# Kernel optimization log

Hardware: AMD Instinct MI355X
Metric: run time of the kernel (lower is better)

## Reference

```python
import jax, jax.numpy as jnp
import numpy as np

B, S, H = 2, 2048, 2048
NH, NKV, HD = 16, 4, 128
SCALING = HD ** -0.5


def rotate_half(x):
    x1, x2 = jnp.split(x, 2, axis=-1)
    return jnp.concatenate((-x2, x1), axis=-1)


def apply_rope(t, cos, sin):
    # t: [B, nh, S, HD]; cos/sin: [B, S, HD] -> unsqueeze head dim
    c = cos[:, None, :, :]
    s = sin[:, None, :, :]
    return t * c + rotate_half(t) * s


def setup_inputs() -> dict:
    key = jax.random.key(0)
    k1, k2, k3, k4, k5 = jax.random.split(key, 5)
    hidden_states = jax.random.normal(k1, (B, S, H), dtype=jnp.float32)
    # real RoPE tables
    inv_freq = 1.0 / (10000.0 ** (jnp.arange(0, HD, 2, dtype=jnp.float32) / HD))
    pos = jnp.arange(S, dtype=jnp.float32)
    freqs = jnp.einsum('s,d->sd', pos, inv_freq)              # [S, HD/2]
    emb = jnp.concatenate((freqs, freqs), axis=-1)            # [S, HD]
    cos = jnp.broadcast_to(jnp.cos(emb)[None], (B, S, HD))
    sin = jnp.broadcast_to(jnp.sin(emb)[None], (B, S, HD))
    # additive causal mask [B, 1, S, S]
    causal = jnp.triu(jnp.full((S, S), -1e9, dtype=jnp.float32), k=1)
    attention_mask = jnp.broadcast_to(causal[None, None], (B, 1, S, S))
    sc = 0.02
    wq = jax.random.normal(k2, (NH * HD, H), dtype=jnp.float32) * sc
    wk = jax.random.normal(k3, (NKV * HD, H), dtype=jnp.float32) * sc
    wv = jax.random.normal(k4, (NKV * HD, H), dtype=jnp.float32) * sc
    wo = jax.random.normal(k5, (H, NH * HD), dtype=jnp.float32) * sc
    return {"hidden_states": hidden_states, "cos": cos, "sin": sin,
            "attention_mask": attention_mask, "wq": wq, "wk": wk, "wv": wv, "wo": wo}


def reference(hidden_states, cos, sin, attention_mask, wq, wk, wv, wo):
    x = hidden_states
    # fused-style QKV projections (nn.Linear: x @ W.T), split heads -> [B, nh, S, HD]
    q = (x @ wq.T).reshape(B, S, NH, HD).transpose(0, 2, 1, 3)
    k = (x @ wk.T).reshape(B, S, NKV, HD).transpose(0, 2, 1, 3)
    v = (x @ wv.T).reshape(B, S, NKV, HD).transpose(0, 2, 1, 3)
    q = apply_rope(q, cos, sin)
    k = apply_rope(k, cos, sin)
    # GQA: repeat KV heads (repeat_kv)
    n_rep = NH // NKV
    k = jnp.repeat(k, n_rep, axis=1)
    v = jnp.repeat(v, n_rep, axis=1)
    scores = jnp.einsum('bhqd,bhkd->bhqk', q, k) * SCALING + attention_mask
    attn = jax.nn.softmax(scores.astype(jnp.float32), axis=-1).astype(q.dtype)
    out = jnp.einsum('bhqk,bhkd->bhqd', attn, v)
    out = out.transpose(0, 2, 1, 3).reshape(B, S, NH * HD)
    out = out @ wo.T
    return (out, attn)
```

## Files before the change

### kernel.cpp

```cpp
#include <hip/hip_runtime.h>
#include <cstdint>
#include <cstddef>

typedef __bf16 bf16;
typedef __attribute__((ext_vector_type(8))) __bf16 bf16x8;
typedef __attribute__((ext_vector_type(4))) __bf16 bf16x4;
typedef __attribute__((ext_vector_type(4))) float f32x4;

constexpr int B_ = 2, S_ = 2048, H_ = 2048, NH_ = 16, NKV_ = 4, HD_ = 128;
constexpr float SCALE_ = 0.08838834764831845f;

#define GLDS16(g, l)                                                        \
  __builtin_amdgcn_global_load_lds(                                         \
      (const __attribute__((address_space(1))) void*)(g),                   \
      (__attribute__((address_space(3))) void*)(l), 16, 0, 0)

#define VMCNT0 asm volatile("s_waitcnt vmcnt(0)" ::: "memory")
#define VMCNT4 asm volatile("s_waitcnt vmcnt(4)" ::: "memory")
#define VMCNT8 asm volatile("s_waitcnt vmcnt(8)" ::: "memory")
#define BAR __builtin_amdgcn_s_barrier()

__global__ void cvt_all(const float* __restrict__ hs, const float* __restrict__ wq,
                        const float* __restrict__ wk, const float* __restrict__ wv,
                        const float* __restrict__ wo, bf16* __restrict__ xb,
                        bf16* __restrict__ w3b, bf16* __restrict__ wob) {
  const int stride = gridDim.x * blockDim.x;
  for (int i = blockIdx.x * blockDim.x + threadIdx.x; i < 4718592; i += stride) {
    const float4* s; bf16x4* d; int j;
    if (i < 2097152)      { s = (const float4*)hs; d = (bf16x4*)xb;            j = i; }
    else if (i < 3145728) { s = (const float4*)wq; d = (bf16x4*)w3b;           j = i - 2097152; }
    else if (i < 3407872) { s = (const float4*)wk; d = (bf16x4*)w3b + 1048576; j = i - 3145728; }
    else if (i < 3670016) { s = (const float4*)wv; d = (bf16x4*)w3b + 1310720; j = i - 3407872; }
    else                  { s = (const float4*)wo; d = (bf16x4*)wob;           j = i - 3670016; }
    float4 v = s[j];
    bf16x4 o;
    o[0] = (bf16)v.x; o[1] = (bf16)v.y; o[2] = (bf16)v.z; o[3] = (bf16)v.w;
    d[j] = o;
  }
}

template <int EPI>
__global__ __launch_bounds__(256, 2) void gemm_bt(const bf16* __restrict__ A,
                                                  const bf16* __restrict__ Bm, int K,
                                                  bf16* __restrict__ qb, bf16* __restrict__ kb,
                                                  bf16* __restrict__ vtb, float* __restrict__ Cout) {
  __shared__ __align__(16) bf16 As[2][128 * 64];
  __shared__ __align__(16) bf16 Bs[2][128 * 64];
  const int tid = threadIdx.x;
  const int lane = tid & 63;
  const int wid = tid >> 6;
  const int fid = blockIdx.y * 32 + blockIdx.x;
  const int nwg = gridDim.y * 32;
  const int swz = (fid & 7) * (nwg >> 3) + (fid >> 3);
  const int m0 = (swz & 31) * 128;
  const int n0 = (swz >> 5) * 128;
  const int wm = (wid >> 1) * 64, wn = (wid & 1) * 64;
  const int r = lane & 15, g = lane >> 4;
  f32x4 acc[4][4] = {};

  auto STAGE = [&](int kt, int cc) {
#pragma unroll
    for (int i = 0; i < 4; ++i) {
      int cb = wid * 256 + i * 64;
      int c64 = cb + lane;
      int row = c64 >> 3, cs = (c64 & 7) ^ (row & 7);
      GLDS16(A + (size_t)(m0 + row) * K + kt + cs * 8, &As[cc][cb * 8]);
      GLDS16(Bm + (size_t)(n0 + row) * K + kt + cs * 8, &Bs[cc][cb * 8]);
    }
  };

  STAGE(0, 0);
  int c = 0;
#pragma unroll 1
  for (int kt = 0; kt < K; kt += 64) {
    if (kt + 64 < K) {
      STAGE(kt + 64, c ^ 1);
      VMCNT8;
    } else {
      VMCNT0;
    }
    BAR;
#pragma unroll
    for (int ks = 0; ks < 2; ++ks) {
      bf16x8 af[4], bfr[4];
#pragma unroll
      for (int fm = 0; fm < 4; ++fm)
        af[fm] = *(const bf16x8*)(&As[c][(wm + fm * 16 + r) * 64 + (((ks * 4 + g) ^ (r & 7)) << 3)]);
#pragma unroll
      for (int fn = 0; fn < 4; ++fn)
        bfr[fn] = *(const bf16x8*)(&Bs[c][(wn + fn * 16 + r) * 64 + (((ks * 4 + g) ^ (r & 7)) << 3)]);
#pragma unroll
      for (int fm = 0; fm < 4; ++fm)
#pragma unroll
        for (int fn = 0; fn < 4; ++fn)
          acc[fm][fn] = __builtin_amdgcn_mfma_f32_16x16x32_bf16(af[fm], bfr[fn], acc[fm][fn], 0, 0, 0);
    }
    BAR;
    c ^= 1;
  }

#pragma unroll
  for (int fm = 0; fm < 4; ++fm)
#pragma unroll
    for (int fn = 0; fn < 4; ++fn)
#pragma unroll
      for (int rr = 0; rr < 4; ++rr) {
        int mm = m0 + wm + fm * 16 + g * 4 + rr;
        int nn = n0 + wn + fn * 16 + r;
        float v = acc[fm][fn][rr];
        if (EPI == 1) {
          Cout[(size_t)mm * 2048 + nn] = v;
        } else {
          int b = mm >> 11, s = mm & (S_ - 1);
          int d = nn & 127;
          if (nn < 2048) {
            int hh = nn >> 7;
            qb[(((size_t)b * NH_ + hh) * S_ + s) * HD_ + d] = (bf16)v;
          } else if (nn < 2560) {
            int hh = (nn - 2048) >> 7;
            kb[(((size_t)b * NKV_ + hh) * S_ + s) * HD_ + d] = (bf16)v;
          } else {
            int hh = (nn - 2560) >> 7;
            vtb[(((size_t)b * NKV_ + hh) * HD_ + d) * S_ + s] = (bf16)v;
          }
        }
      }
}

__global__ void rope_kernel(bf16* __restrict__ qb, bf16* __restrict__ kb,
                            const float* __restrict__ cosp, const float* __restrict__ sinp) {
  const int NQ = B_ * NH_ * S_;
  const int NK = B_ * NKV_ * S_;
  const int tot = (NQ + NK) * 8;
  int t = blockIdx.x * blockDim.x + threadIdx.x;
  if (t >= tot) return;
  const int oct = t & 7, rid = t >> 3;
  bf16* base;
  int b, s;
  if (rid < NQ) {
    base = qb + (size_t)rid * HD_;
    s = rid & (S_ - 1);
    b = rid >> 15;
  } else {
    int r2 = rid - NQ;
    base = kb + (size_t)r2 * HD_;
    s = r2 & (S_ - 1);
    b = r2 >> 13;
  }
  const int d = oct * 8;
  const float* cp = cosp + ((size_t)b * S_ + s) * HD_ + d;
  const float* sp = sinp + ((size_t)b * S_ + s) * HD_ + d;
  float4 c0 = *(const float4*)cp, c1 = *(const float4*)(cp + 4);
  float4 s0 = *(const float4*)sp, s1 = *(const float4*)(sp + 4);
  float cc[8] = {c0.x, c0.y, c0.z, c0.w, c1.x, c1.y, c1.z, c1.w};
  float ss[8] = {s0.x, s0.y, s0.z, s0.w, s1.x, s1.y, s1.z, s1.w};
  bf16x8 x1 = *(const bf16x8*)(base + d);
  bf16x8 x2 = *(const bf16x8*)(base + d + 64);
  bf16x8 o1, o2;
#pragma unroll
  for (int i = 0; i < 8; ++i) {
    float a = (float)x1[i], bb = (float)x2[i];
    o1[i] = (bf16)(a * cc[i] - bb * ss[i]);
    o2[i] = (bf16)(bb * cc[i] + a * ss[i]);
  }
  *(bf16x8*)(base + d) = o1;
  *(bf16x8*)(base + d + 64) = o2;
}

__global__ __launch_bounds__(256, 2) void attn_kernel(const bf16* __restrict__ qb,
                                                      const bf16* __restrict__ kb,
                                                      const bf16* __restrict__ vtb,
                                                      bf16* __restrict__ aob,
                                                      float* __restrict__ attn_out) {
  __shared__ __align__(16) bf16 Ks[2][64 * 128];
  __shared__ __align__(16) bf16 Vs[2][128 * 64];
  __shared__ __align__(16) bf16 Ps[64 * 64];
  const int bid = (blockIdx.x & 7) * 64 + (blockIdx.x >> 3);
  const int p = bid & 15;
  const int h = (bid >> 4) & 15;
  const int b = bid >> 8;
  const int kh = h >> 2;
  const int tid = threadIdx.x, lane = tid & 63, wid = tid >> 6;
  const int r = lane & 15, g = lane >> 4;

  const bf16* kbase = kb + ((size_t)b * NKV_ + kh) * S_ * HD_;
  const bf16* vbase = vtb + ((size_t)b * NKV_ + kh) * (size_t)HD_ * S_;
  const size_t ahead = (size_t)(b * NH_ + h) * S_;

  auto stageK = [&](int kt, int cc) {
#pragma unroll
    for (int i = 0; i < 4; ++i) {
      int base = i * 256 + wid * 64;
      int idx = base + lane;
      int row = idx >> 4, ch = (idx & 15) ^ (row & 7);
      GLDS16(kbase + (size_t)(kt * 64 + row) * HD_ + ch * 8, &Ks[cc][base * 8]);
    }
  };
  auto stageV = [&](int kt, int cc) {
#pragma unroll
    for (int i = 0; i < 4; ++i) {
      int base = i * 256 + wid * 64;
      int idx = base + lane;
      int row = idx >> 3, ch = (idx & 7) ^ (row & 7);
      GLDS16(vbase + (size_t)row * S_ + kt * 64 + ch * 8, &Vs[cc][base * 8]);
    }
  };

  int zc = 0;

#pragma unroll 1
  for (int sbi = 0; sbi < 2; ++sbi) {
    const int qt = sbi ? 31 - p : p;
    const int q0 = qt * 64;
    const int nt = qt + 1;
    const bf16* qsrc = qb + ((size_t)(b * NH_ + h) * S_ + q0) * HD_;

    bf16x8 qreg[4];
#pragma unroll
    for (int ks = 0; ks < 4; ++ks)
      qreg[ks] = *(const bf16x8*)(qsrc + (wid * 16 + r) * HD_ + ks * 32 + g * 8);

    float lsum = 0.f;
    stageK(0, 0);
    VMCNT0; BAR;
    int c = 0;
#pragma unroll 1
    for (int kt = 0; kt < nt; ++kt) {
      if (kt + 1 < nt) stageK(kt + 1, c ^ 1);
      const bool dz = (zc <= 30);
      if (dz) {
        int qtz, ktz;
        if (zc < 31 - p) { qtz = p; ktz = p + 1 + zc; }
        else             { qtz = 31 - p; ktz = zc + 1; }
        float* zdst = attn_out + (ahead + qtz * 64) * S_ + ktz * 64;
        float4 z = {0.f, 0.f, 0.f, 0.f};
#pragma unroll
        for (int i = 0; i < 4; ++i) {
          int idx = i * 256 + tid;
          *(float4*)(zdst + (size_t)(idx >> 4) * S_ + (idx & 15) * 4) = z;
        }
        ++zc;
      }
      f32x4 sacc[4] = {};
      __builtin_amdgcn_s_setprio(1);
#pragma unroll
      for (int ks = 0; ks < 4; ++ks)
#pragma unroll
        for (int fn = 0; fn < 4; ++fn) {
          bf16x8 kk = *(const bf16x8*)(&Ks[c][(fn * 16 + r) * 128 + (((ks * 4 + g) ^ (r & 7)) << 3)]);
          sacc[fn] = __builtin_amdgcn_mfma_f32_16x16x32_bf16(kk, qreg[ks], sacc[fn], 0, 0, 0);
        }
      __builtin_amdgcn_s_setprio(0);
      float ts = 0.f;
      if (kt == nt - 1) {
#pragma unroll
        for (int fn = 0; fn < 4; ++fn)
#pragma unroll
          for (int rr = 0; rr < 4; ++rr) {
            bool msk = (fn * 16 + g * 4 + rr) > (wid * 16 + r);
            ts += msk ? 0.f : __expf(sacc[fn][rr] * SCALE_);
          }
      } else {
#pragma unroll
        for (int fn = 0; fn < 4; ++fn)
#pragma unroll
          for (int rr = 0; rr < 4; ++rr) ts += __expf(sacc[fn][rr] * SCALE_);
      }
      ts += __shfl_xor(ts, 16);
      ts += __shfl_xor(ts, 32);
      lsum += ts;
      if (dz) { VMCNT4; } else { VMCNT0; }
      BAR;
      c ^= 1;
    }
    const float rl = 1.0f / lsum;

    f32x4 oacc[8] = {};
    const size_t arow0 = (ahead + q0) * S_;
    stageK(0, 0);
    stageV(0, 0);
    VMCNT0; BAR;
    c = 0;
#pragma unroll 1
    for (int kt = 0; kt < nt; ++kt) {
      if (kt + 1 < nt) { stageK(kt + 1, c ^ 1); stageV(kt + 1, c ^ 1); }
      const int k0 = kt * 64;
      f32x4 sacc[4] = {};
      __builtin_amdgcn_s_setprio(1);
#pragma unroll
      for (int ks = 0; ks < 4; ++ks)
#pragma unroll
        for (int fn = 0; fn < 4; ++fn) {
          bf16x8 kk = *(const bf16x8*)(&Ks[c][(fn * 16 + r) * 128 + (((ks * 4 + g) ^ (r & 7)) << 3)]);
          sacc[fn] = __builtin_amdgcn_mfma_f32_16x16x32_bf16(kk, qreg[ks], sacc[fn], 0, 0, 0);
        }
      __builtin_amdgcn_s_setprio(0);
      const int prow = (wid * 16 + r) * 64;
      if (kt == nt - 1) {
#pragma unroll
        for (int fn = 0; fn < 4; ++fn) {
          bf16x4 pk;
#pragma unroll
          for (int rr = 0; rr < 4; ++rr) {
            bool msk = (fn * 16 + g * 4 + rr) > (wid * 16 + r);
            pk[rr] = (bf16)(msk ? 0.f : __expf(sacc[fn][rr] * SCALE_) * rl);
          }
          *(bf16x4*)(&Ps[prow + ((((fn << 1) | (g >> 1)) ^ (r & 7)) << 3) + ((g & 1) << 2)]) = pk;
        }
      } else {
#pragma unroll
        for (int fn = 0; fn < 4; ++fn) {
          bf16x4 pk;
#pragma unroll
          for (int rr = 0; rr < 4; ++rr)
            pk[rr] = (bf16)(__expf(sacc[fn][rr] * SCALE_) * rl);
          *(bf16x4*)(&Ps[prow + ((((fn << 1) | (g >> 1)) ^ (r & 7)) << 3) + ((g & 1) << 2)]) = pk;
        }
      }
      {
        const int trow = tid >> 2, tcb = (tid & 3) * 16;
        float* dst = attn_out + arow0 + (size_t)trow * S_ + k0 + tcb;
        int ch0 = (tid & 3) * 2;
        bf16x8 p0 = *(const bf16x8*)(&Ps[trow * 64 + ((ch0 ^ (trow & 7)) << 3)]);
        bf16x8 p1 = *(const bf16x8*)(&Ps[trow * 64 + (((ch0 + 1) ^ (trow & 7)) << 3)]);
        float4 o0 = {(float)p0[0], (float)p0[1], (float)p0[2], (float)p0[3]};
        float4 o1 = {(float)p0[4], (float)p0[5], (float)p0[6], (float)p0[7]};
        float4 o2 = {(float)p1[0], (float)p1[1], (float)p1[2], (float)p1[3]};
        float4 o3 = {(float)p1[4], (float)p1[5], (float)p1[6], (float)p1[7]};
        *(float4*)(dst) = o0;
        *(float4*)(dst + 4) = o1;
        *(float4*)(dst + 8) = o2;
        *(float4*)(dst + 12) = o3;
      }
      __builtin_amdgcn_s_setprio(1);
#pragma unroll
      for (int ks = 0; ks < 2; ++ks) {
        bf16x8 pa = *(const bf16x8*)(&Ps[prow + (((ks * 4 + g) ^ (r & 7)) << 3)]);
#pragma unroll
        for (int fn = 0; fn < 8; ++fn) {
          bf16x8 vv = *(const bf16x8*)(&Vs[c][(fn * 16 + r) * 64 + (((ks * 4 + g) ^ (r & 7)) << 3)]);
          oacc[fn] = __builtin_amdgcn_mfma_f32_16x16x32_bf16(pa, vv, oacc[fn], 0, 0, 0);
        }
      }
      __builtin_amdgcn_s_setprio(0);
      VMCNT4; BAR;
      c ^= 1;
    }

#pragma unroll
    for (int fn = 0; fn < 8; ++fn)
#pragma unroll
      for (int rr = 0; rr < 4; ++rr) {
        int q = q0 + wid * 16 + g * 4 + rr;
        aob[((size_t)b * S_ + q) * 2048 + h * HD_ + fn * 16 + r] = (bf16)oacc[fn][rr];
      }
  }
}

extern "C" void kernel_launch(void* const* d_in, const int* in_sizes, int n_in,
                              void* d_out, int out_size, void* d_ws, size_t ws_size,
                              hipStream_t stream) {
  const float* hidden = (const float*)d_in[0];
  const float* cosp = (const float*)d_in[1];
  const float* sinp = (const float*)d_in[2];
  const float* wq = (const float*)d_in[4];
  const float* wk = (const float*)d_in[5];
  const float* wv = (const float*)d_in[6];
  const float* wo = (const float*)d_in[7];
  float* out = (float*)d_out;
  float* attn = out + (size_t)B_ * S_ * H_;

  char* ws = (char*)d_ws;
  bf16* xb  = (bf16*)(ws);
  bf16* w3b = (bf16*)(ws + (16ull << 20));
  bf16* wob = (bf16*)(ws + (28ull << 20));
  bf16* qb  = (bf16*)(ws + (36ull << 20));
  bf16* kb  = (bf16*)(ws + (52ull << 20));
  bf16* vtb = (bf16*)(ws + (56ull << 20));
  bf16* aob = (bf16*)(ws + (60ull << 20));

  cvt_all<<<2048, 256, 0, stream>>>(hidden, wq, wk, wv, wo, xb, w3b, wob);
  gemm_bt<0><<<dim3(32, 24), 256, 0, stream>>>(xb, w3b, 2048, qb, kb, vtb, nullptr);
  rope_kernel<<<2560, 256, 0, stream>>>(qb, kb, cosp, sinp);
  attn_kernel<<<512, 256, 0, stream>>>(qb, kb, vtb, aob, attn);
  gemm_bt<1><<<dim3(32, 16), 256, 0, stream>>>(aob, wob, 2048, nullptr, nullptr, nullptr, out);
}
```

Baseline: 349.7 us.

## Fuse Q RoPE into attention and single-buffer the projection GEMM

RoPE for Q is now applied in registers inside the attention kernel when the Q fragments are loaded, and the standalone rope kernel only rotates K. This removes a full read-modify-write pass over the Q tensor. Separately, the GEMM drops its double-buffered LDS pipeline for a single buffer with a full wait and two barriers per k-step, and relaxes the launch bounds. That halves LDS use but gives up overlap of global loads with MFMA work.

```diff
diff --git a/kernel.cpp b/kernel.cpp
--- a/kernel.cpp
+++ b/kernel.cpp
@@ -17,7 +17,6 @@
 
 #define VMCNT0 asm volatile("s_waitcnt vmcnt(0)" ::: "memory")
 #define VMCNT4 asm volatile("s_waitcnt vmcnt(4)" ::: "memory")
-#define VMCNT8 asm volatile("s_waitcnt vmcnt(8)" ::: "memory")
 #define BAR __builtin_amdgcn_s_barrier()
 
 __global__ void cvt_all(const float* __restrict__ hs, const float* __restrict__ wq,
@@ -40,12 +39,12 @@
 }
 
 template <int EPI>
-__global__ __launch_bounds__(256, 2) void gemm_bt(const bf16* __restrict__ A,
-                                                  const bf16* __restrict__ Bm, int K,
-                                                  bf16* __restrict__ qb, bf16* __restrict__ kb,
-                                                  bf16* __restrict__ vtb, float* __restrict__ Cout) {
-  __shared__ __align__(16) bf16 As[2][128 * 64];
-  __shared__ __align__(16) bf16 Bs[2][128 * 64];
+__global__ __launch_bounds__(256) void gemm_bt(const bf16* __restrict__ A,
+                                               const bf16* __restrict__ Bm, int K,
+                                               bf16* __restrict__ qb, bf16* __restrict__ kb,
+                                               bf16* __restrict__ vtb, float* __restrict__ Cout) {
+  __shared__ __align__(16) bf16 As[128 * 64];
+  __shared__ __align__(16) bf16 Bs[128 * 64];
   const int tid = threadIdx.x;
   const int lane = tid & 63;
   const int wid = tid >> 6;
@@ -58,45 +57,34 @@
   const int r = lane & 15, g = lane >> 4;
   f32x4 acc[4][4] = {};
 
-  auto STAGE = [&](int kt, int cc) {
+#pragma unroll 1
+  for (int kt = 0; kt < K; kt += 64) {
+    __syncthreads();
 #pragma unroll
     for (int i = 0; i < 4; ++i) {
       int cb = wid * 256 + i * 64;
       int c64 = cb + lane;
       int row = c64 >> 3, cs = (c64 & 7) ^ (row & 7);
-      GLDS16(A + (size_t)(m0 + row) * K + kt + cs * 8, &As[cc][cb * 8]);
-      GLDS16(Bm + (size_t)(n0 + row) * K + kt + cs * 8, &Bs[cc][cb * 8]);
-    }
-  };
-
-  STAGE(0, 0);
-  int c = 0;
-#pragma unroll 1
-  for (int kt = 0; kt < K; kt += 64) {
-    if (kt + 64 < K) {
-      STAGE(kt + 64, c ^ 1);
-      VMCNT8;
-    } else {
-      VMCNT0;
-    }
-    BAR;
+      GLDS16(A + (size_t)(m0 + row) * K + kt + cs * 8, As + cb * 8);
+      GLDS16(Bm + (size_t)(n0 + row) * K + kt + cs * 8, Bs + cb * 8);
+    }
+    VMCNT0;
+    __syncthreads();
 #pragma unroll
     for (int ks = 0; ks < 2; ++ks) {
       bf16x8 af[4], bfr[4];
 #pragma unroll
       for (int fm = 0; fm < 4; ++fm)
-        af[fm] = *(const bf16x8*)(&As[c][(wm + fm * 16 + r) * 64 + (((ks * 4 + g) ^ (r & 7)) << 3)]);
+        af[fm] = *(const bf16x8*)(As + (wm + fm * 16 + r) * 64 + (((ks * 4 + g) ^ (r & 7)) << 3));
 #pragma unroll
       for (int fn = 0; fn < 4; ++fn)
-        bfr[fn] = *(const bf16x8*)(&Bs[c][(wn + fn * 16 + r) * 64 + (((ks * 4 + g) ^ (r & 7)) << 3)]);
+        bfr[fn] = *(const bf16x8*)(Bs + (wn + fn * 16 + r) * 64 + (((ks * 4 + g) ^ (r & 7)) << 3));
 #pragma unroll
       for (int fm = 0; fm < 4; ++fm)
 #pragma unroll
         for (int fn = 0; fn < 4; ++fn)
           acc[fm][fn] = __builtin_amdgcn_mfma_f32_16x16x32_bf16(af[fm], bfr[fn], acc[fm][fn], 0, 0, 0);
     }
-    BAR;
-    c ^= 1;
   }
 
 #pragma unroll
@@ -127,26 +115,15 @@
       }
 }
 
-__global__ void rope_kernel(bf16* __restrict__ qb, bf16* __restrict__ kb,
-                            const float* __restrict__ cosp, const float* __restrict__ sinp) {
-  const int NQ = B_ * NH_ * S_;
+__global__ void rope_k_kernel(bf16* __restrict__ kb, const float* __restrict__ cosp,
+                              const float* __restrict__ sinp) {
   const int NK = B_ * NKV_ * S_;
-  const int tot = (NQ + NK) * 8;
   int t = blockIdx.x * blockDim.x + threadIdx.x;
-  if (t >= tot) return;
+  if (t >= NK * 8) return;
   const int oct = t & 7, rid = t >> 3;
-  bf16* base;
-  int b, s;
-  if (rid < NQ) {
-    base = qb + (size_t)rid * HD_;
-    s = rid & (S_ - 1);
-    b = rid >> 15;
-  } else {
-    int r2 = rid - NQ;
-    base = kb + (size_t)r2 * HD_;
-    s = r2 & (S_ - 1);
-    b = r2 >> 13;
-  }
+  bf16* base = kb + (size_t)rid * HD_;
+  const int s = rid & (S_ - 1);
+  const int b = rid >> 13;
   const int d = oct * 8;
   const float* cp = cosp + ((size_t)b * S_ + s) * HD_ + d;
   const float* sp = sinp + ((size_t)b * S_ + s) * HD_ + d;
@@ -170,6 +147,8 @@
 __global__ __launch_bounds__(256, 2) void attn_kernel(const bf16* __restrict__ qb,
                                                       const bf16* __restrict__ kb,
                                                       const bf16* __restrict__ vtb,
+                                                      const float* __restrict__ cosp,
+                                                      const float* __restrict__ sinp,
                                                       bf16* __restrict__ aob,
                                                       float* __restrict__ attn_out) {
   __shared__ __align__(16) bf16 Ks[2][64 * 128];
@@ -216,9 +195,29 @@
     const bf16* qsrc = qb + ((size_t)(b * NH_ + h) * S_ + q0) * HD_;
 
     bf16x8 qreg[4];
-#pragma unroll
-    for (int ks = 0; ks < 4; ++ks)
-      qreg[ks] = *(const bf16x8*)(qsrc + (wid * 16 + r) * HD_ + ks * 32 + g * 8);
+    {
+      const int srow = q0 + wid * 16 + r;
+#pragma unroll
+      for (int ks = 0; ks < 4; ++ks)
+        qreg[ks] = *(const bf16x8*)(qsrc + (wid * 16 + r) * HD_ + ks * 32 + g * 8);
+      const float* cp = cosp + ((size_t)b * S_ + srow) * HD_;
+      const float* sp = sinp + ((size_t)b * S_ + srow) * HD_;
+#pragma unroll
+      for (int hf = 0; hf < 2; ++hf) {
+        const int d0 = hf * 32 + g * 8;
+        float4 ca = *(const float4*)(cp + d0), cb2 = *(const float4*)(cp + d0 + 4);
+        float4 sa = *(const float4*)(sp + d0), sb2 = *(const float4*)(sp + d0 + 4);
+        float cc[8] = {ca.x, ca.y, ca.z, ca.w, cb2.x, cb2.y, cb2.z, cb2.w};
+        float ss[8] = {sa.x, sa.y, sa.z, sa.w, sb2.x, sb2.y, sb2.z, sb2.w};
+        bf16x8 lo = qreg[hf], hi = qreg[hf + 2];
+#pragma unroll
+        for (int i = 0; i < 8; ++i) {
+          float a = (float)lo[i], bb = (float)hi[i];
+          qreg[hf][i] = (bf16)(a * cc[i] - bb * ss[i]);
+          qreg[hf + 2][i] = (bf16)(bb * cc[i] + a * ss[i]);
+        }
+      }
+    }
 
     float lsum = 0.f;
     stageK(0, 0);
@@ -381,7 +380,7 @@
 
   cvt_all<<<2048, 256, 0, stream>>>(hidden, wq, wk, wv, wo, xb, w3b, wob);
   gemm_bt<0><<<dim3(32, 24), 256, 0, stream>>>(xb, w3b, 2048, qb, kb, vtb, nullptr);
-  rope_kernel<<<2560, 256, 0, stream>>>(qb, kb, cosp, sinp);
-  attn_kernel<<<512, 256, 0, stream>>>(qb, kb, vtb, aob, attn);
+  rope_k_kernel<<<512, 256, 0, stream>>>(kb, cosp, sinp);
+  attn_kernel<<<512, 256, 0, stream>>>(qb, kb, vtb, cosp, sinp, aob, attn);
   gemm_bt<1><<<dim3(32, 16), 256, 0, stream>>>(aob, wob, 2048, nullptr, nullptr, nullptr, out);
 }
```

Result: no change. 347.8 us (-0.5%).
